# Kernel tuning notes

Hardware: AMD Instinct MI355X
Metric: run time of the kernel (lower is better)

The kernel has to match this reference:

```python
import jax, jax.numpy as jnp
import numpy as np
from jax import lax

B, N, C_IN = 16, 4096, 64
RATIO, R, K = 0.25, 0.2, 32
MLP = [64, 64, 128]
EPS = 1e-5  # BatchNorm eps


def setup_inputs() -> dict:
    key = jax.random.key(0)
    ks = jax.random.split(key, 8)
    inp = {
        "x": jax.random.normal(ks[0], (B, N, C_IN), jnp.float32),
        "pos": jax.random.uniform(ks[1], (B, N, 3), jnp.float32),
    }
    dims = [C_IN + 3] + MLP  # [67, 64, 64, 128]
    for i in range(3):
        scale = float(np.sqrt(2.0 / dims[i]))
        inp[f"W{i+1}"] = jax.random.normal(ks[2 + i], (dims[i], dims[i + 1]), jnp.float32) * scale
        inp[f"g{i+1}"] = jnp.ones((dims[i + 1],), jnp.float32)   # BN gamma
        inp[f"b{i+1}"] = jnp.zeros((dims[i + 1],), jnp.float32)  # BN beta
        inp[f"rm{i+1}"] = jnp.zeros((dims[i + 1],), jnp.float32) # BN running mean
        inp[f"rv{i+1}"] = jnp.ones((dims[i + 1],), jnp.float32)  # BN running var
    return inp


def _fps(pos, m):
    """Farthest point sampling on one cloud pos [N,3]; deterministic start at 0."""
    n = pos.shape[0]

    def body(i, carry):
        mind, idxs = carry
        last = pos[idxs[i - 1]]
        mind = jnp.minimum(mind, jnp.sum((pos - last) ** 2, axis=-1))
        idxs = idxs.at[i].set(jnp.argmax(mind).astype(jnp.int32))
        return mind, idxs

    mind0 = jnp.full((n,), 1e10, pos.dtype)
    idxs0 = jnp.zeros((m,), jnp.int32)
    _, idxs = lax.fori_loop(1, m, body, (mind0, idxs0))
    return idxs


def reference(x, pos, W1, g1, b1, rm1, rv1, W2, g2, b2, rm2, rv2, W3, g3, b3, rm3, rv3):
    bb, n, _ = pos.shape
    m = int(round(n * RATIO))
    # ---- FPS (indices are constants wrt grads) ----
    idx = jax.vmap(lambda p: _fps(p, m))(lax.stop_gradient(pos))        # [B,M]
    cpos = jnp.take_along_axis(pos, idx[..., None], axis=1)             # [B,M,3]
    # ---- ball query: first K points (in index order) within radius R ----
    d2 = jnp.sum((cpos[:, :, None, :] - pos[:, None, :, :]) ** 2, -1)   # [B,M,N]
    score = jnp.where(d2 <= R * R, n - jnp.arange(n, dtype=jnp.int32), 0)
    topv = lax.top_k(score, K)[0]                                       # [B,M,K]
    valid = topv > 0  # centroid itself is always within radius -> >=1 valid
    nidx = jnp.where(valid, n - topv, 0)                                # [B,M,K]
    # ---- gather neighbors + relative positions ----
    flat = nidx.reshape(bb, m * K)
    x_j = jnp.take_along_axis(x, flat[..., None], axis=1).reshape(bb, m, K, -1)
    pos_j = jnp.take_along_axis(pos, flat[..., None], axis=1).reshape(bb, m, K, 3)
    h = jnp.concatenate([x_j, pos_j - cpos[:, :, None, :]], axis=-1)    # [B,M,K,67]
    # ---- shared MLP: Linear(no bias) -> BN(eval) -> ReLU, x3 ----
    for (W, g, b, rm, rv) in ((W1, g1, b1, rm1, rv1), (W2, g2, b2, rm2, rv2), (W3, g3, b3, rm3, rv3)):
        h = jax.nn.relu((h @ W - rm) * (g * lax.rsqrt(rv + EPS)) + b)
    # ---- scatter-max aggregation over neighbors ----
    h = jnp.where(valid[..., None], h, -jnp.inf)
    x_out = jnp.max(h, axis=2)                                          # [B,M,128]
    return x_out, cpos
```

## Files before the change

### kernel.cpp

```cpp
#include <hip/hip_runtime.h>
#include <hip/hip_bf16.h>
#include <float.h>
#include <math.h>

#define BATCH 16
#define NPTS  4096
#define CIN   64
#define MCENT 1024
#define KNB   32
#define OUT_X (BATCH * MCENT * 128)

__device__ __forceinline__ float f_sub(float a, float b){ float r; asm("v_sub_f32 %0, %1, %2" : "=v"(r) : "v"(a), "v"(b)); return r; }
__device__ __forceinline__ float f_mul(float a, float b){ float r; asm("v_mul_f32 %0, %1, %2" : "=v"(r) : "v"(a), "v"(b)); return r; }
__device__ __forceinline__ float f_add(float a, float b){ float r; asm("v_add_f32 %0, %1, %2" : "=v"(r) : "v"(a), "v"(b)); return r; }

__device__ __forceinline__ float dist2_exact(float px, float py, float pz,
                                             float lx, float ly, float lz) {
    float dx = f_sub(px, lx), dy = f_sub(py, ly), dz = f_sub(pz, lz);
    return f_add(f_add(f_mul(dx, dx), f_mul(dy, dy)), f_mul(dz, dz));
}

template <int CTRL>
__device__ __forceinline__ float dpp_max(float x) {
    int xi = __float_as_int(x);
    int yi = __builtin_amdgcn_update_dpp(xi, xi, CTRL, 0xF, 0xF, false);
    return fmaxf(x, __int_as_float(yi));
}
__device__ __forceinline__ float wave_max_f32(float v) {
    v = dpp_max<0xB1>(v);
    v = dpp_max<0x4E>(v);
    v = dpp_max<0x141>(v);
    v = dpp_max<0x140>(v);
    int s = __builtin_amdgcn_ds_swizzle(__float_as_int(v), 0x401F);
    v = fmaxf(v, __int_as_float(s));
    v = fmaxf(v, __shfl_xor(v, 32));
    return v;
}

__global__ __launch_bounds__(512, 1) void fps_kernel(
    const float* __restrict__ pos, float* __restrict__ cpos)
{
    __shared__ float spx[NPTS], spy[NPTS], spz[NPTS];
    __shared__ __align__(16) float swmax[8];
    __shared__ int widxslot[2];
    __shared__ int widxarr[MCENT];

    const int b = blockIdx.x;
    const int t = threadIdx.x;
    const float* pb = pos + (size_t)b * NPTS * 3;

    float px[8], py[8], pz[8], mind[8];
    {
        const float4* src = (const float4*)(pb + t * 24);
        float v[24];
#pragma unroll
        for (int q = 0; q < 6; ++q) {
            float4 f = src[q];
            v[q * 4 + 0] = f.x; v[q * 4 + 1] = f.y; v[q * 4 + 2] = f.z; v[q * 4 + 3] = f.w;
        }
#pragma unroll
        for (int j = 0; j < 8; ++j) {
            int n = t * 8 + j;
            px[j] = v[j * 3 + 0]; py[j] = v[j * 3 + 1]; pz[j] = v[j * 3 + 2];
            spx[n] = px[j]; spy[n] = py[j]; spz[n] = pz[j];
            mind[j] = 1e10f;
        }
    }
    if (t == 0) { widxslot[0] = 0x7FFFFFFF; widxslot[1] = 0x7FFFFFFF; widxarr[0] = 0; }
    __syncthreads();

    int w = 0;
    for (int i = 1; i < MCENT; ++i) {
        float lx = spx[w], ly = spy[w], lz = spz[w];
        float tmax = -1.0f;
#pragma unroll
        for (int j = 0; j < 8; ++j) {
            float d = dist2_exact(px[j], py[j], pz[j], lx, ly, lz);
            mind[j] = fminf(mind[j], d);
            tmax = fmaxf(tmax, mind[j]);
        }
        float wmax = wave_max_f32(tmax);
        if ((t & 63) == 0) swmax[t >> 6] = wmax;
        __syncthreads();
        float4 m0 = *(const float4*)&swmax[0];
        float4 m1 = *(const float4*)&swmax[4];
        float gmax = fmaxf(fmaxf(fmaxf(m0.x, m0.y), fmaxf(m0.z, m0.w)),
                           fmaxf(fmaxf(m1.x, m1.y), fmaxf(m1.z, m1.w)));
        if (t == 0) widxslot[(i + 1) & 1] = 0x7FFFFFFF;
        if (tmax == gmax) {
            int cand = 0x7FFFFFFF;
#pragma unroll
            for (int j = 7; j >= 0; --j)
                if (mind[j] == gmax) cand = t * 8 + j;
            atomicMin(&widxslot[i & 1], cand);
        }
        __syncthreads();
        w = widxslot[i & 1];
        if (t == 0) widxarr[i] = w;
    }
    __syncthreads();
#pragma unroll
    for (int e = 0; e < 2; ++e) {
        int c = t + e * 512;
        int src = widxarr[c];
        float* cp = cpos + ((size_t)b * MCENT + c) * 3;
        cp[0] = spx[src]; cp[1] = spy[src]; cp[2] = spz[src];
    }
}

__global__ __launch_bounds__(256) void ballq_kernel(
    const float* __restrict__ pos, const float* __restrict__ cpos,
    int* __restrict__ nidx)
{
    const int wid  = blockIdx.x * 4 + (threadIdx.x >> 6);
    const int lane = threadIdx.x & 63;
    const int b    = wid >> 10;
    const float* pb = pos + (size_t)b * NPTS * 3;
    const float cx = cpos[wid * 3 + 0];
    const float cy = cpos[wid * 3 + 1];
    const float cz = cpos[wid * 3 + 2];
    const float R2 = (float)(0.2 * 0.2);
    int* outp = nidx + (size_t)wid * KNB;

    int cnt = 0;
    for (int j0 = 0; j0 < NPTS; j0 += 64) {
        int j = j0 + lane;
        float x = pb[j * 3 + 0], y = pb[j * 3 + 1], z = pb[j * 3 + 2];
        float d = dist2_exact(x, y, z, cx, cy, cz);
        bool valid = (d <= R2);
        unsigned long long msk = __ballot(valid);
        if (valid) {
            int rank = cnt + __popcll(msk & ((1ull << lane) - 1ull));
            if (rank < KNB) outp[rank] = j;
        }
        cnt += __popcll(msk);
        if (cnt >= KNB) break;
    }
    int nv = cnt < KNB ? cnt : KNB;
    if (lane >= nv && lane < KNB) outp[lane] = -1;
}

__global__ __launch_bounds__(256, 1) void mlp_kernel(
    const float* __restrict__ x, const float* __restrict__ pos,
    const float* __restrict__ W1, const float* __restrict__ g1, const float* __restrict__ b1,
    const float* __restrict__ rm1, const float* __restrict__ rv1,
    const float* __restrict__ W2, const float* __restrict__ g2, const float* __restrict__ b2,
    const float* __restrict__ rm2, const float* __restrict__ rv2,
    const float* __restrict__ W3, const float* __restrict__ g3, const float* __restrict__ b3,
    const float* __restrict__ rm3, const float* __restrict__ rv3,
    const float* __restrict__ cpos, const int* __restrict__ nidx,
    float* __restrict__ out)
{
    __shared__ float hbuf[256 * 69];
    __shared__ float sscale[256], sbias[256];

    const int t   = threadIdx.x;
    const int g   = t >> 5;
    const int k   = t & 31;
    const int cid0 = blockIdx.x * 8;
    const int cid  = cid0 + g;
    const int b    = cid >> 10;

    {
        float gg, bb, rm, rv;
        if (t < 64)       { gg = g1[t];     bb = b1[t];     rm = rm1[t];     rv = rv1[t]; }
        else if (t < 128) { int c = t - 64;  gg = g2[c]; bb = b2[c]; rm = rm2[c]; rv = rv2[c]; }
        else              { int c = t - 128; gg = g3[c]; bb = b3[c]; rm = rm3[c]; rv = rv3[c]; }
        float s = gg / sqrtf(rv + 1e-5f);
        sscale[t] = s;
        sbias[t]  = bb - rm * s;
    }

    const int j = nidx[(size_t)cid * KNB + k];
    const bool valid = (j >= 0);
    float* hrow = &hbuf[t * 69];
    if (valid) {
        const float* xr = x + ((size_t)b * NPTS + j) * CIN;
#pragma unroll
        for (int q = 0; q < 16; ++q) {
            float4 v = ((const float4*)xr)[q];
            hrow[q * 4 + 0] = v.x; hrow[q * 4 + 1] = v.y;
            hrow[q * 4 + 2] = v.z; hrow[q * 4 + 3] = v.w;
        }
        const float* pr = pos + ((size_t)b * NPTS + j) * 3;
        hrow[64] = f_sub(pr[0], cpos[cid * 3 + 0]);
        hrow[65] = f_sub(pr[1], cpos[cid * 3 + 1]);
        hrow[66] = f_sub(pr[2], cpos[cid * 3 + 2]);
    } else {
        for (int q = 0; q < 67; ++q) hrow[q] = 0.f;
    }
    __syncthreads();

    float acc[64];
#pragma unroll
    for (int c = 0; c < 64; ++c) acc[c] = 0.f;
#pragma unroll 2
    for (int kk = 0; kk < 67; ++kk) {
        float hv = hrow[kk];
        const float* wr = W1 + kk * 64;
#pragma unroll
        for (int c = 0; c < 64; ++c) acc[c] = fmaf(hv, wr[c], acc[c]);
    }
#pragma unroll
    for (int c = 0; c < 64; ++c)
        hrow[c] = fmaxf(fmaf(acc[c], sscale[c], sbias[c]), 0.f);

#pragma unroll
    for (int c = 0; c < 64; ++c) acc[c] = 0.f;
#pragma unroll 2
    for (int kk = 0; kk < 64; ++kk) {
        float hv = hrow[kk];
        const float* wr = W2 + kk * 64;
#pragma unroll
        for (int c = 0; c < 64; ++c) acc[c] = fmaf(hv, wr[c], acc[c]);
    }
#pragma unroll
    for (int c = 0; c < 64; ++c)
        hrow[c] = fmaxf(fmaf(acc[c], sscale[64 + c], sbias[64 + c]), 0.f);

    float acc3[128];
#pragma unroll
    for (int c = 0; c < 128; ++c) acc3[c] = 0.f;
#pragma unroll 2
    for (int kk = 0; kk < 64; ++kk) {
        float hv = hrow[kk];
        const float* wr = W3 + kk * 128;
#pragma unroll
        for (int c = 0; c < 128; ++c) acc3[c] = fmaf(hv, wr[c], acc3[c]);
    }
#pragma unroll
    for (int c = 0; c < 128; ++c) {
        float v = fmaxf(fmaf(acc3[c], sscale[128 + c], sbias[128 + c]), 0.f);
        acc3[c] = valid ? v : -FLT_MAX;
    }

#pragma unroll
    for (int half = 0; half < 2; ++half) {
        __syncthreads();
#pragma unroll
        for (int c = 0; c < 64; ++c) hbuf[t * 69 + c] = acc3[half * 64 + c];
        __syncthreads();
#pragma unroll
        for (int e0 = 0; e0 < 2; ++e0) {
            int e  = t + e0 * 256;
            int gg = e >> 6, c = e & 63;
            float mv = -FLT_MAX;
#pragma unroll
            for (int kk2 = 0; kk2 < 32; ++kk2)
                mv = fmaxf(mv, hbuf[(gg * 32 + kk2) * 69 + c]);
            out[((size_t)(cid0 + gg)) * 128 + half * 64 + c] = mv;
        }
    }
}

extern "C" void kernel_launch(void* const* d_in, const int* in_sizes, int n_in,
                              void* d_out, int out_size, void* d_ws, size_t ws_size,
                              hipStream_t stream) {
    const float* x   = (const float*)d_in[0];
    const float* pos = (const float*)d_in[1];
    const float* W1  = (const float*)d_in[2];
    const float* g1  = (const float*)d_in[3];
    const float* b1  = (const float*)d_in[4];
    const float* rm1 = (const float*)d_in[5];
    const float* rv1 = (const float*)d_in[6];
    const float* W2  = (const float*)d_in[7];
    const float* g2  = (const float*)d_in[8];
    const float* b2  = (const float*)d_in[9];
    const float* rm2 = (const float*)d_in[10];
    const float* rv2 = (const float*)d_in[11];
    const float* W3  = (const float*)d_in[12];
    const float* g3  = (const float*)d_in[13];
    const float* b3  = (const float*)d_in[14];
    const float* rm3 = (const float*)d_in[15];
    const float* rv3 = (const float*)d_in[16];

    float* out  = (float*)d_out;
    float* cpos = out + OUT_X;
    int*   nidx = (int*)d_ws;

    fps_kernel<<<dim3(BATCH), dim3(512), 0, stream>>>(pos, cpos);
    ballq_kernel<<<dim3(BATCH * MCENT / 4), dim3(256), 0, stream>>>(pos, cpos, nidx);
    mlp_kernel<<<dim3(BATCH * MCENT / 8), dim3(256), 0, stream>>>(
        x, pos, W1, g1, b1, rm1, rv1, W2, g2, b2, rm2, rv2,
        W3, g3, b3, rm3, rv3, cpos, nidx, out);
}
```

Before: 1.174 ms.

## Use packed 64-bit atomicMax argmax to drop one barrier per FPS step

The FPS loop now packs (max distance, inverted index) into one 64-bit key, and each wave's max holders do an atomicMax into a rotating 4-entry LDS slot. This removes the per-wave max staging and one of the two block barriers per iteration. The cross-lane 32 shuffle in the wave reduction is replaced with v_permlane32_swap, and the per-thread max becomes a tree. The cost is 64-bit LDS atomics from every wave each step, plus slot rotation that must stay correct across iterations. Ties rely on non-negative float bit ordering.

```diff
diff --git a/kernel.cpp b/kernel.cpp
--- a/kernel.cpp
+++ b/kernel.cpp
@@ -33,16 +33,16 @@
     v = dpp_max<0x140>(v);
     int s = __builtin_amdgcn_ds_swizzle(__float_as_int(v), 0x401F);
     v = fmaxf(v, __int_as_float(s));
-    v = fmaxf(v, __shfl_xor(v, 32));
-    return v;
+    float a = v, b = v;
+    asm("v_permlane32_swap_b32 %0, %1" : "+v"(a), "+v"(b));
+    return fmaxf(a, b);
 }
 
 __global__ __launch_bounds__(512, 1) void fps_kernel(
     const float* __restrict__ pos, float* __restrict__ cpos)
 {
     __shared__ float spx[NPTS], spy[NPTS], spz[NPTS];
-    __shared__ __align__(16) float swmax[8];
-    __shared__ int widxslot[2];
+    __shared__ unsigned long long slot[4];
     __shared__ int widxarr[MCENT];
 
     const int b = blockIdx.x;
@@ -66,36 +66,37 @@
             mind[j] = 1e10f;
         }
     }
-    if (t == 0) { widxslot[0] = 0x7FFFFFFF; widxslot[1] = 0x7FFFFFFF; widxarr[0] = 0; }
+    if (t == 0) {
+        slot[0] = 0ull; slot[1] = 0ull; slot[2] = 0ull; slot[3] = 0ull;
+        widxarr[0] = 0;
+    }
     __syncthreads();
 
     int w = 0;
     for (int i = 1; i < MCENT; ++i) {
         float lx = spx[w], ly = spy[w], lz = spz[w];
-        float tmax = -1.0f;
 #pragma unroll
         for (int j = 0; j < 8; ++j) {
             float d = dist2_exact(px[j], py[j], pz[j], lx, ly, lz);
             mind[j] = fminf(mind[j], d);
-            tmax = fmaxf(tmax, mind[j]);
-        }
+        }
+        float tmax = fmaxf(fmaxf(fmaxf(mind[0], mind[1]), fmaxf(mind[2], mind[3])),
+                           fmaxf(fmaxf(mind[4], mind[5]), fmaxf(mind[6], mind[7])));
         float wmax = wave_max_f32(tmax);
-        if ((t & 63) == 0) swmax[t >> 6] = wmax;
+        if (tmax == wmax) {
+            int cand = 0;
+#pragma unroll
+            for (int j = 7; j >= 0; --j)
+                if (mind[j] == wmax) cand = t * 8 + j;
+            unsigned long long key =
+                ((unsigned long long)__float_as_uint(wmax) << 32) |
+                (unsigned)(NPTS - 1 - cand);
+            atomicMax(&slot[i & 3], key);
+        }
+        if (t == 0) slot[(i + 2) & 3] = 0ull;
         __syncthreads();
-        float4 m0 = *(const float4*)&swmax[0];
-        float4 m1 = *(const float4*)&swmax[4];
-        float gmax = fmaxf(fmaxf(fmaxf(m0.x, m0.y), fmaxf(m0.z, m0.w)),
-                           fmaxf(fmaxf(m1.x, m1.y), fmaxf(m1.z, m1.w)));
-        if (t == 0) widxslot[(i + 1) & 1] = 0x7FFFFFFF;
-        if (tmax == gmax) {
-            int cand = 0x7FFFFFFF;
-#pragma unroll
-            for (int j = 7; j >= 0; --j)
-                if (mind[j] == gmax) cand = t * 8 + j;
-            atomicMin(&widxslot[i & 1], cand);
-        }
-        __syncthreads();
-        w = widxslot[i & 1];
+        unsigned long long win = slot[i & 3];
+        w = (NPTS - 1) - (int)(unsigned)(win & 0xFFFFFFFFull);
         if (t == 0) widxarr[i] = w;
     }
     __syncthreads();
```

Measured after the change: 1.120 ms. 1.05x faster.
